# Performance work log

Measured on AMD Instinct MI355X. Metric: run time of the kernel, lower is better.

The kernel has to match this reference:

```python
import jax, jax.numpy as jnp
import numpy as np

B, N, D, D_OUT = 8, 2048, 1024, 1024

def setup_inputs() -> dict:
    key = jax.random.key(0)
    k1, k2, k3, k4, k5 = jax.random.split(key, 5)
    x = jax.random.normal(k1, (B, N, D), dtype=jnp.float32)
    # nn.Linear params: weight [out, in], bias [out]
    W_attn = jax.random.normal(k2, (D, D), dtype=jnp.float32) / np.sqrt(D)
    b_attn = jax.random.normal(k3, (D,), dtype=jnp.float32) * 0.01
    W_out = jax.random.normal(k4, (D_OUT, D), dtype=jnp.float32) / np.sqrt(D)
    b_out = jax.random.normal(k5, (D_OUT,), dtype=jnp.float32) * 0.01
    return {"x": x, "W_attn": W_attn, "b_attn": b_attn, "W_out": W_out, "b_out": b_out}

def reference(x, W_attn, b_attn, W_out, b_out):
    # query = x; key = attention_linear(x); value = output_linear(x)
    key = jnp.einsum('bnd,kd->bnk', x, W_attn) + b_attn   # [B,N,D]
    value = jnp.einsum('bnd,od->bno', x, W_out) + b_out   # [B,N,D_OUT]
    scale = 1.0 / np.sqrt(x.shape[-1]).astype(np.float32)
    scores = jnp.einsum('bqd,bkd->bqk', x, key) * scale   # [B,N,N]
    attn = jax.nn.softmax(scores, axis=-1)
    return jnp.einsum('bqk,bko->bqo', attn, value)        # [B,N,D_OUT]
```

## Files before the change

kernel.cpp:

```cpp
#include <hip/hip_runtime.h>
#include <hip/hip_bf16.h>
#include <cstdio>

typedef __bf16 bf16_t;
typedef __bf16 bf16x8 __attribute__((ext_vector_type(8)));
typedef __bf16 bf16x4 __attribute__((ext_vector_type(4)));
typedef float  f32x16 __attribute__((ext_vector_type(16)));

#define TILE_E (256 * 64)

__global__ __launch_bounds__(256)
void cvt_all(const float* __restrict__ x,  bf16_t* __restrict__ xb,  int nX,
             const float* __restrict__ Wa, bf16_t* __restrict__ Wab,
             const float* __restrict__ Wo, bf16_t* __restrict__ Wob, int nW)
{
    const int nT = nX + 2 * nW;
    for (int i = (blockIdx.x * 256 + threadIdx.x) * 4; i < nT; i += gridDim.x * 256 * 4) {
        const float* src; bf16_t* dst; int off;
        if (i < nX)            { src = x;  dst = xb;  off = i; }
        else if (i < nX + nW)  { src = Wa; dst = Wab; off = i - nX; }
        else                   { src = Wo; dst = Wob; off = i - nX - nW; }
        const float4 v = *(const float4*)(src + off);
        bf16x4 o;
        o[0] = (bf16_t)v.x; o[1] = (bf16_t)v.y; o[2] = (bf16_t)v.z; o[3] = (bf16_t)v.w;
        *(bf16x4*)(dst + off) = o;
    }
}


template<int K>
__device__ __forceinline__ void stage_half(
    const bf16_t* __restrict__ src, bf16_t* lds_tile,
    int half, int kt, int w, int l)
{
    const int r0 = half * 128 + w * 8 + (l >> 3);
    const int c8 = ((l & 7) ^ (l >> 3) ^ ((w & 3) << 1)) * 8;
#pragma unroll
    for (int rr = 0; rr < 2; rr++) {
        __builtin_amdgcn_global_load_lds(
            (const __attribute__((address_space(1))) void*)
                (src + (size_t)(r0 + rr * 64) * K + (size_t)kt * 64 + c8),
            (__attribute__((address_space(3))) void*)
                (lds_tile + (half * 128 + rr * 64 + w * 8) * 64),
            16, 0, 0);
    }
}

#define RDF_A(f, ks) (*(const bf16x8*)&sAc[(aoff + (f) * 32 + l31) * 64 + ((((ks) * 2 + l5) ^ swz) * 8)])
#define RDF_B(f, ks) (*(const bf16x8*)&sBc[(boff + (f) * 32 + l31) * 64 + ((((ks) * 2 + l5) ^ swz) * 8)])

#define MFMA_Q(AR, BV, MB, NB)                                             \
    _Pragma("unroll") for (int ks = 0; ks < 4; ks++)                       \
    _Pragma("unroll") for (int mi = 0; mi < 2; mi++)                       \
        acc[(MB) + mi][NB] = __builtin_amdgcn_mfma_f32_32x32x16_bf16(      \
            AR[mi][ks], BV[ks], acc[(MB) + mi][NB], 0, 0, 0);

#define LGKM0_FENCE                                        \
    asm volatile("s_waitcnt lgkmcnt(0)" ::: "memory");     \
    __builtin_amdgcn_sched_barrier(0);

template<int K>
__device__ __forceinline__ void gemm256_core(
    const bf16_t* __restrict__ Ab, const bf16_t* __restrict__ Bb,
    f32x16 (&acc)[4][2], int w, int l, int wm, int wn)
{
    __shared__ bf16_t sA[2 * TILE_E];
    __shared__ bf16_t sB[2 * TILE_E];
    constexpr int NKT = K / 64;

    const int l31 = l & 31, l5 = l >> 5;
    const int swz = (l & 7) ^ ((l >> 2) & 6);
    const int aoff = wm * 128, boff = wn * 64;

    stage_half<K>(Ab, sA, 0, 0, w, l);
    stage_half<K>(Bb, sB, 0, 0, w, l);
    stage_half<K>(Ab, sA, 1, 0, w, l);
    stage_half<K>(Bb, sB, 1, 0, w, l);
    asm volatile("s_waitcnt vmcnt(0)" ::: "memory");
    __builtin_amdgcn_s_barrier();

    bf16x8 arA[2][4], arB[2][4], bl[4], bh[4];

    for (int t = 0; t < NKT; ++t) {
        bf16_t* sAc = sA + (t & 1) * TILE_E;
        bf16_t* sBc = sB + (t & 1) * TILE_E;
        bf16_t* sAn = sA + ((t + 1) & 1) * TILE_E;
        bf16_t* sBn = sB + ((t + 1) & 1) * TILE_E;
        const bool pf = (t + 1 < NKT);

#pragma unroll
        for (int mi = 0; mi < 2; mi++)
#pragma unroll
            for (int ks = 0; ks < 4; ks++) arA[mi][ks] = RDF_A(mi, ks);
#pragma unroll
        for (int ks = 0; ks < 4; ks++) bl[ks] = RDF_B(0, ks);
        if (pf) {
            stage_half<K>(Ab, sAn, 0, t + 1, w, l);
            stage_half<K>(Bb, sBn, 0, t + 1, w, l);
        }
        asm volatile("s_waitcnt lgkmcnt(8)" ::: "memory");
        __builtin_amdgcn_s_barrier();
        LGKM0_FENCE
        __builtin_amdgcn_s_setprio(1);
        MFMA_Q(arA, bl, 0, 0)
        __builtin_amdgcn_s_setprio(0);
        __builtin_amdgcn_s_barrier();

#pragma unroll
        for (int ks = 0; ks < 4; ks++) bh[ks] = RDF_B(1, ks);
        if (pf) {
            stage_half<K>(Ab, sAn, 1, t + 1, w, l);
            stage_half<K>(Bb, sBn, 1, t + 1, w, l);
        }
        __builtin_amdgcn_s_barrier();
        LGKM0_FENCE
        __builtin_amdgcn_s_setprio(1);
        MFMA_Q(arA, bh, 0, 1)
        __builtin_amdgcn_s_setprio(0);
        __builtin_amdgcn_s_barrier();

#pragma unroll
        for (int mi = 0; mi < 2; mi++)
#pragma unroll
            for (int ks = 0; ks < 4; ks++) arB[mi][ks] = RDF_A(2 + mi, ks);
        __builtin_amdgcn_s_barrier();
        LGKM0_FENCE
        __builtin_amdgcn_s_setprio(1);
        MFMA_Q(arB, bl, 2, 0)
        __builtin_amdgcn_s_setprio(0);
        __builtin_amdgcn_s_barrier();

        __builtin_amdgcn_s_setprio(1);
        MFMA_Q(arB, bh, 2, 1)
        __builtin_amdgcn_s_setprio(0);
        if (pf) {
            asm volatile("s_waitcnt vmcnt(0)" ::: "memory");
            __builtin_amdgcn_s_barrier();
        }
    }
}

#define ACC_INIT(acc)                                            \
    _Pragma("unroll") for (int i = 0; i < 4; i++)                \
    _Pragma("unroll") for (int j = 0; j < 2; j++)                \
    _Pragma("unroll") for (int e = 0; e < 16; e++) acc[i][j][e] = 0.f;

__global__ __launch_bounds__(512, 2)
void gemm_kv8(const bf16_t* __restrict__ xb,
              const bf16_t* __restrict__ Wa, const bf16_t* __restrict__ Wo,
              const float* __restrict__ ba, const float* __restrict__ bo,
              bf16_t* __restrict__ key, bf16_t* __restrict__ vT)
{
    constexpr int K = 1024, Nn = 2048, Dd = 1024;
    const int tid = threadIdx.x;
    const int w = tid >> 6, l = tid & 63;
    const int wm = w >> 2, wn = w & 3;

    const int bid = blockIdx.x;
    const int id  = (bid & 7) * 64 + (bid >> 3);
    const int b   = id >> 6;
    const int rest = id & 63;
    const int tm  = rest & 7;
    const int tn  = rest >> 3;
    const bool isK = tn < 4;

    const bf16_t* Ab = xb + (size_t)b * Nn * K + (size_t)tm * 256 * K;
    const bf16_t* Bb = isK ? (Wa + (size_t)tn * 256 * K)
                           : (Wo + (size_t)(tn - 4) * 256 * K);

    f32x16 acc[4][2];
    ACC_INIT(acc)
    gemm256_core<K>(Ab, Bb, acc, w, l, wm, wn);

    const int l31 = l & 31, l5 = l >> 5;
    if (isK) {
#pragma unroll
        for (int n = 0; n < 2; n++) {
            const int cg = (tn & 3) * 256 + wn * 64 + n * 32 + l31;
            const float bv = ba[cg];
#pragma unroll
            for (int m = 0; m < 4; m++)
#pragma unroll
                for (int rg = 0; rg < 4; rg++) {
                    const int rowg = tm * 256 + wm * 128 + m * 32 + rg * 8 + 4 * l5;
                    bf16_t* p = key + (size_t)b * Nn * Dd + (size_t)rowg * Dd + cg;
#pragma unroll
                    for (int j = 0; j < 4; j++)
                        p[(size_t)j * Dd] = (bf16_t)(acc[m][n][rg * 4 + j] + bv);
                }
        }
    } else {
#pragma unroll
        for (int n = 0; n < 2; n++) {
            const int cg = (tn & 3) * 256 + wn * 64 + n * 32 + l31;
            const float bv = bo[cg];
#pragma unroll
            for (int m = 0; m < 4; m++)
#pragma unroll
                for (int rg = 0; rg < 4; rg++) {
                    const int rowg = tm * 256 + wm * 128 + m * 32 + rg * 8 + 4 * l5;
                    bf16x4 pk;
#pragma unroll
                    for (int j = 0; j < 4; j++) pk[j] = (bf16_t)(acc[m][n][rg * 4 + j] + bv);
                    *(bf16x4*)(vT + (size_t)b * Dd * Nn + (size_t)cg * Nn + rowg) = pk;
                }
        }
    }
}

__global__ __launch_bounds__(512, 2)
void gemm_scores8(const bf16_t* __restrict__ xb, const bf16_t* __restrict__ key,
                  bf16_t* __restrict__ S, float* __restrict__ rowpart)
{
    constexpr int K = 1024, Nn = 2048;
    const int tid = threadIdx.x;
    const int w = tid >> 6, l = tid & 63;
    const int wm = w >> 2, wn = w & 3;

    const int bid = blockIdx.x;
    const int id  = (bid & 7) * 64 + (bid >> 3);
    const int b   = id >> 6;
    const int rest = id & 63;
    const int tm  = rest & 7;
    const int tn  = rest >> 3;

    const bf16_t* Ab = xb  + (size_t)b * Nn * K + (size_t)tm * 256 * K;
    const bf16_t* Bb = key + (size_t)b * Nn * K + (size_t)tn * 256 * K;

    f32x16 acc[4][2];
    ACC_INIT(acc)
    gemm256_core<K>(Ab, Bb, acc, w, l, wm, wn);

    const int l31 = l & 31, l5 = l >> 5;
#pragma unroll
    for (int m = 0; m < 4; m++) {
        float part[4][4];
#pragma unroll
        for (int rg = 0; rg < 4; rg++)
#pragma unroll
            for (int j = 0; j < 4; j++) part[rg][j] = 0.f;
#pragma unroll
        for (int n = 0; n < 2; n++) {
            const int cg = tn * 256 + wn * 64 + n * 32 + l31;
#pragma unroll
            for (int rg = 0; rg < 4; rg++) {
                const int rowg = tm * 256 + wm * 128 + m * 32 + rg * 8 + 4 * l5;
                bf16_t* p = S + (size_t)b * Nn * Nn + (size_t)rowg * Nn + cg;
#pragma unroll
                for (int j = 0; j < 4; j++) {
                    const float e = __expf(acc[m][n][rg * 4 + j] * 0.03125f);
                    part[rg][j] += e;
                    p[(size_t)j * Nn] = (bf16_t)e;
                }
            }
        }
#pragma unroll
        for (int rg = 0; rg < 4; rg++)
#pragma unroll
            for (int j = 0; j < 4; j++) {
                float v = part[rg][j];
#pragma unroll
                for (int off = 16; off >= 1; off >>= 1)
                    v += __shfl_xor(v, off);
                if (l31 == 0) {
                    const int rowg = tm * 256 + wm * 128 + m * 32 + rg * 8 + 4 * l5 + j;
                    rowpart[((size_t)b * 2048 + rowg) * 32 + tn * 4 + wn] = v;
                }
            }
    }
}

__global__ __launch_bounds__(512, 2)
void gemm_out8(const bf16_t* __restrict__ P, const bf16_t* __restrict__ vT,
               const float* __restrict__ rowpart, float* __restrict__ out)
{
    constexpr int K = 2048, Nn = 2048, Dd = 1024;
    __shared__ float invS[256];

    const int tid = threadIdx.x;
    const int w = tid >> 6, l = tid & 63;
    const int wm = w >> 2, wn = w & 3;

    const int bid = blockIdx.x;
    const int id  = (bid & 7) * 32 + (bid >> 3);
    const int b   = id >> 5;
    const int rest = id & 31;
    const int tm  = rest & 7;
    const int tn  = rest >> 3;

    if (tid < 256) {
        const float* rp = rowpart + ((size_t)b * 2048 + tm * 256 + tid) * 32;
        float s = 0.f;
#pragma unroll
        for (int i = 0; i < 32; i++) s += rp[i];
        invS[tid] = 1.f / s;
    }

    const bf16_t* Ab = P  + (size_t)b * Nn * Nn + (size_t)tm * 256 * Nn;
    const bf16_t* Bb = vT + (size_t)b * Dd * Nn + (size_t)tn * 256 * Nn;

    f32x16 acc[4][2];
    ACC_INIT(acc)
    gemm256_core<K>(Ab, Bb, acc, w, l, wm, wn);

    const int l31 = l & 31, l5 = l >> 5;
#pragma unroll
    for (int n = 0; n < 2; n++) {
        const int cg = tn * 256 + wn * 64 + n * 32 + l31;
#pragma unroll
        for (int m = 0; m < 4; m++)
#pragma unroll
            for (int rg = 0; rg < 4; rg++) {
                const int rl = wm * 128 + m * 32 + rg * 8 + 4 * l5;
                float* p = out + (size_t)b * Nn * Dd + (size_t)(tm * 256 + rl) * Dd + cg;
#pragma unroll
                for (int j = 0; j < 4; j++)
                    p[(size_t)j * Dd] = acc[m][n][rg * 4 + j] * invS[rl + j];
            }
    }
}

extern "C" void kernel_launch(void* const* d_in, const int* in_sizes, int n_in,
                              void* d_out, int out_size, void* d_ws, size_t ws_size,
                              hipStream_t stream)
{
    const int Bn = 8, Nn = 2048, Dd = 1024;

    const float* x  = (const float*)d_in[0];
    const float* Wa = (const float*)d_in[1];
    const float* ba = (const float*)d_in[2];
    const float* Wo = (const float*)d_in[3];
    const float* bo = (const float*)d_in[4];
    float* out = (float*)d_out;

    const size_t nX = (size_t)Bn * Nn * Dd;
    const size_t nW = (size_t)Dd * Dd;
    const size_t nS = (size_t)Bn * Nn * Nn;
    const size_t nR = (size_t)Bn * 2048 * 32;

    bf16_t* xb  = (bf16_t*)d_ws;
    bf16_t* Wab = xb + nX;
    bf16_t* Wob = Wab + nW;
    bf16_t* key = Wob + nW;
    bf16_t* vT  = key + nX;
    bf16_t* S   = vT + nX;
    float* rowpart = (float*)(S + nS);
    const size_t needed = (nX * 3 + nW * 2 + nS) * sizeof(bf16_t) + nR * sizeof(float);
    if (ws_size < needed)
        fprintf(stderr, "kernel_launch: ws too small: have %zu need %zu\n", ws_size, needed);

    cvt_all<<<dim3(18432), dim3(256), 0, stream>>>(x, xb, (int)nX, Wa, Wab, Wo, Wob, (int)nW);

    gemm_kv8<<<dim3(512), dim3(512), 0, stream>>>(xb, Wab, Wob, ba, bo, key, vT);

    gemm_scores8<<<dim3(512), dim3(512), 0, stream>>>(xb, key, S, rowpart);

    gemm_out8<<<dim3(256), dim3(512), 0, stream>>>(S, vT, rowpart, out);
}
```

Before: 363.4 us.

## Software-pipeline LDS fragment reads and drop intra-iteration barriers in GEMM core

Restructures the bf16 GEMM main loop so each wave prefetches the next tile's A and B-low fragments right after the end-of-iteration barrier. The B-high and second A fragments are issued ahead of the MFMA groups that use them, with partial lgkmcnt waits instead of full drains. Most per-quarter s_barriers are removed and replaced by scheduling barriers, leaving one workgroup barrier per k-tile. The aim is to overlap LDS reads with MFMA work and cut synchronisation stalls. The risk is higher register pressure and getting the hand-counted waitcnt values wrong.

```diff
diff --git a/kernel.cpp b/kernel.cpp
--- a/kernel.cpp
+++ b/kernel.cpp
@@ -46,8 +46,8 @@
     }
 }
 
-#define RDF_A(f, ks) (*(const bf16x8*)&sAc[(aoff + (f) * 32 + l31) * 64 + ((((ks) * 2 + l5) ^ swz) * 8)])
-#define RDF_B(f, ks) (*(const bf16x8*)&sBc[(boff + (f) * 32 + l31) * 64 + ((((ks) * 2 + l5) ^ swz) * 8)])
+#define RDF(buf, off, f, ks) \
+    (*(const bf16x8*)&buf[((off) + (f) * 32 + l31) * 64 + ((((ks) * 2 + l5) ^ swz) * 8)])
 
 #define MFMA_Q(AR, BV, MB, NB)                                             \
     _Pragma("unroll") for (int ks = 0; ks < 4; ks++)                       \
@@ -55,9 +55,7 @@
         acc[(MB) + mi][NB] = __builtin_amdgcn_mfma_f32_32x32x16_bf16(      \
             AR[mi][ks], BV[ks], acc[(MB) + mi][NB], 0, 0, 0);
 
-#define LGKM0_FENCE                                        \
-    asm volatile("s_waitcnt lgkmcnt(0)" ::: "memory");     \
-    __builtin_amdgcn_sched_barrier(0);
+#define SBAR __builtin_amdgcn_sched_barrier(0);
 
 template<int K>
 __device__ __forceinline__ void gemm256_core(
@@ -78,8 +76,17 @@
     stage_half<K>(Bb, sB, 1, 0, w, l);
     asm volatile("s_waitcnt vmcnt(0)" ::: "memory");
     __builtin_amdgcn_s_barrier();
+    SBAR
 
     bf16x8 arA[2][4], arB[2][4], bl[4], bh[4];
+
+#pragma unroll
+    for (int mi = 0; mi < 2; mi++)
+#pragma unroll
+        for (int ks = 0; ks < 4; ks++) arA[mi][ks] = RDF(sA, aoff, mi, ks);
+#pragma unroll
+    for (int ks = 0; ks < 4; ks++) bl[ks] = RDF(sB, boff, 0, ks);
+    SBAR
 
     for (int t = 0; t < NKT; ++t) {
         bf16_t* sAc = sA + (t & 1) * TILE_E;
@@ -88,54 +95,54 @@
         bf16_t* sBn = sB + ((t + 1) & 1) * TILE_E;
         const bool pf = (t + 1 < NKT);
 
-#pragma unroll
-        for (int mi = 0; mi < 2; mi++)
-#pragma unroll
-            for (int ks = 0; ks < 4; ks++) arA[mi][ks] = RDF_A(mi, ks);
-#pragma unroll
-        for (int ks = 0; ks < 4; ks++) bl[ks] = RDF_B(0, ks);
         if (pf) {
             stage_half<K>(Ab, sAn, 0, t + 1, w, l);
             stage_half<K>(Bb, sBn, 0, t + 1, w, l);
         }
-        asm volatile("s_waitcnt lgkmcnt(8)" ::: "memory");
-        __builtin_amdgcn_s_barrier();
-        LGKM0_FENCE
+#pragma unroll
+        for (int ks = 0; ks < 4; ks++) bh[ks] = RDF(sBc, boff, 1, ks);
+        SBAR
+        asm volatile("s_waitcnt lgkmcnt(4)" ::: "memory");
+        SBAR
         __builtin_amdgcn_s_setprio(1);
         MFMA_Q(arA, bl, 0, 0)
         __builtin_amdgcn_s_setprio(0);
-        __builtin_amdgcn_s_barrier();
-
-#pragma unroll
-        for (int ks = 0; ks < 4; ks++) bh[ks] = RDF_B(1, ks);
+        SBAR
+
         if (pf) {
             stage_half<K>(Ab, sAn, 1, t + 1, w, l);
             stage_half<K>(Bb, sBn, 1, t + 1, w, l);
         }
-        __builtin_amdgcn_s_barrier();
-        LGKM0_FENCE
+#pragma unroll
+        for (int mi = 0; mi < 2; mi++)
+#pragma unroll
+            for (int ks = 0; ks < 4; ks++) arB[mi][ks] = RDF(sAc, aoff, 2 + mi, ks);
+        SBAR
+        asm volatile("s_waitcnt lgkmcnt(8)" ::: "memory");
+        SBAR
         __builtin_amdgcn_s_setprio(1);
         MFMA_Q(arA, bh, 0, 1)
         __builtin_amdgcn_s_setprio(0);
-        __builtin_amdgcn_s_barrier();
-
-#pragma unroll
-        for (int mi = 0; mi < 2; mi++)
-#pragma unroll
-            for (int ks = 0; ks < 4; ks++) arB[mi][ks] = RDF_A(2 + mi, ks);
-        __builtin_amdgcn_s_barrier();
-        LGKM0_FENCE
+        SBAR
+
+        asm volatile("s_waitcnt lgkmcnt(0)" ::: "memory");
+        SBAR
         __builtin_amdgcn_s_setprio(1);
         MFMA_Q(arB, bl, 2, 0)
-        __builtin_amdgcn_s_setprio(0);
-        __builtin_amdgcn_s_barrier();
-
-        __builtin_amdgcn_s_setprio(1);
         MFMA_Q(arB, bh, 2, 1)
         __builtin_amdgcn_s_setprio(0);
+
         if (pf) {
             asm volatile("s_waitcnt vmcnt(0)" ::: "memory");
             __builtin_amdgcn_s_barrier();
+            SBAR
+#pragma unroll
+            for (int mi = 0; mi < 2; mi++)
+#pragma unroll
+                for (int ks = 0; ks < 4; ks++) arA[mi][ks] = RDF(sAn, aoff, mi, ks);
+#pragma unroll
+            for (int ks = 0; ks < 4; ks++) bl[ks] = RDF(sBn, boff, 0, ks);
+            SBAR
         }
     }
 }
```

New measurement: 371.8 us. 1.02x slower.
